# Performance work log

Hardware: AMD Instinct MI355X
Metric: run time of the kernel (lower is better)

The kernel has to match this reference:

```python
import jax, jax.numpy as jnp
import numpy as np

N, E = 100000, 600000
IN, HID, OUT, ED = 128, 128, 64, 32


def _gine_conv(x, src, dst, edge_feats, We, be, Wa, ba, Wb, bb):
    # GINEConv: msg = relu(x_j + Linear(edge_attr)); out = MLP((1+eps)*x + sum msg), eps=0
    e = edge_feats @ We + be                      # [E, C]
    msg = jax.nn.relu(x[src] + e)                 # gather + edge-add
    agg = jax.ops.segment_sum(msg, dst, num_segments=x.shape[0])
    h = x + agg                                   # eps = 0
    return jax.nn.relu(h @ Wa + ba) @ Wb + bb     # 2-layer MLP


def setup_inputs() -> dict:
    key = jax.random.key(0)
    ks = jax.random.split(key, 20)
    g = lambda k, shp, fan: jax.random.normal(k, shp, jnp.float32) * (1.0 / np.sqrt(fan))
    return {
        "x": jax.random.normal(ks[0], (N, IN), jnp.float32),
        "edge_index": jax.random.randint(ks[1], (2, E), 0, N, dtype=jnp.int32),
        "edge_feats": jax.random.normal(ks[2], (E, ED), jnp.float32),
        # conv1: edge lin (ED->IN), nn1 (IN->HID->HID)
        "We1": g(ks[3], (ED, IN), ED), "be1": jnp.zeros((IN,), jnp.float32),
        "W1a": g(ks[4], (IN, HID), IN), "b1a": jnp.zeros((HID,), jnp.float32),
        "W1b": g(ks[5], (HID, HID), HID), "b1b": jnp.zeros((HID,), jnp.float32),
        # conv2: edge lin (ED->HID), nn2 (HID->HID->HID)
        "We2": g(ks[6], (ED, HID), ED), "be2": jnp.zeros((HID,), jnp.float32),
        "W2a": g(ks[7], (HID, HID), HID), "b2a": jnp.zeros((HID,), jnp.float32),
        "W2b": g(ks[8], (HID, HID), HID), "b2b": jnp.zeros((HID,), jnp.float32),
        # heads
        "Wfc1": g(ks[9], (HID, HID), HID), "bfc1": jnp.zeros((HID,), jnp.float32),
        "Wfc2": g(ks[10], (HID, OUT), HID), "bfc2": jnp.zeros((OUT,), jnp.float32),
    }


def reference(x, edge_index, edge_feats,
              We1, be1, W1a, b1a, W1b, b1b,
              We2, be2, W2a, b2a, W2b, b2b,
              Wfc1, bfc1, Wfc2, bfc2):
    src, dst = edge_index[0], edge_index[1]  # source_to_target flow
    h = _gine_conv(x, src, dst, edge_feats, We1, be1, W1a, b1a, W1b, b1b)
    h = jnp.tanh(h)                          # dropout: eval-mode identity
    h = _gine_conv(h, src, dst, edge_feats, We2, be2, W2a, b2a, W2b, b2b)
    h = jnp.tanh(h)
    h = jnp.tanh(h @ Wfc1 + bfc1)
    return h @ Wfc2 + bfc2
```

## Files before the change

kernel.cpp:

```cpp
#include <hip/hip_runtime.h>
#include <hip/hip_fp16.h>
#include <math.h>

#define N_NODES 100000
#define N_EDGES 600000
#define NB_SCAN ((N_NODES + 1023) / 1024)

typedef unsigned short u16;
typedef __bf16 bf16x8 __attribute__((ext_vector_type(8)));
typedef float  f32x4  __attribute__((ext_vector_type(4)));

__device__ __forceinline__ u16 f2bf(float f) {
    union { float f; unsigned u; } c; c.f = f;
    unsigned u = c.u + 0x7fffu + ((c.u >> 16) & 1u);
    return (u16)(u >> 16);
}
__device__ __forceinline__ float bf2f(u16 h) {
    union { unsigned u; float f; } c; c.u = ((unsigned)h) << 16;
    return c.f;
}
__device__ __forceinline__ float fast_tanh(float x) {
    float e = __expf(2.0f * x);
    return 1.0f - 2.0f * __builtin_amdgcn_rcpf(e + 1.0f);
}

__global__ void hist_k(const int* __restrict__ dst, int* __restrict__ counts,
                       int* __restrict__ rank)
{
    int e = blockIdx.x * 256 + threadIdx.x;
    if (e < N_EDGES) rank[e] = atomicAdd(&counts[dst[e]], 1);
}

__global__ void scan_a_k(const int* __restrict__ counts, int* __restrict__ row_ptr,
                         int* __restrict__ blockSums)
{
    __shared__ int s[256];
    const int t = threadIdx.x;
    const int base = blockIdx.x * 1024 + t * 4;
    int c[4];
#pragma unroll
    for (int j = 0; j < 4; ++j) c[j] = (base + j < N_NODES) ? counts[base + j] : 0;
    const int tot = c[0] + c[1] + c[2] + c[3];
    s[t] = tot;
    __syncthreads();
    for (int off = 1; off < 256; off <<= 1) {
        int v = (t >= off) ? s[t - off] : 0;
        __syncthreads();
        s[t] += v;
        __syncthreads();
    }
    int run = s[t] - tot;
#pragma unroll
    for (int j = 0; j < 4; ++j) {
        if (base + j < N_NODES) row_ptr[base + j] = run;
        run += c[j];
    }
    if (t == 255) blockSums[blockIdx.x] = s[255];
}

__global__ void scan_b_k(const int* __restrict__ blockSums, int* __restrict__ blockOffs)
{
    if (threadIdx.x == 0) {
        int run = 0;
        for (int b = 0; b < NB_SCAN; ++b) { blockOffs[b] = run; run += blockSums[b]; }
    }
}

__global__ void scan_c_k(int* __restrict__ row_ptr, const int* __restrict__ blockOffs)
{
    int i = blockIdx.x * 256 + threadIdx.x;
    if (i < N_NODES) row_ptr[i] += blockOffs[i >> 10];
    if (i == 0) row_ptr[N_NODES] = N_EDGES;
}

__global__ void scatter_k(const int* __restrict__ src, const int* __restrict__ dst,
                          const int* __restrict__ row_ptr, const int* __restrict__ rank,
                          int* __restrict__ perm, int* __restrict__ src_sorted,
                          int* __restrict__ dst_sorted)
{
    int e = blockIdx.x * 256 + threadIdx.x;
    if (e < N_EDGES) {
        int pos = row_ptr[dst[e]] + rank[e];
        perm[pos] = e;
        src_sorted[pos] = src[e];
        dst_sorted[pos] = dst[e];
    }
}

__global__ void nzero_k(const int* __restrict__ row_ptr, float* __restrict__ agg)
{
    const int idx = blockIdx.x * 256 + threadIdx.x;
    const int n = idx >> 5;
    if (n >= N_NODES) return;
    const int rs = row_ptr[n], re = row_ptr[n + 1];
    const bool interior = (rs < re) && ((rs >> 6) == ((re - 1) >> 6));
    if (!interior) {
        const int c = (idx & 31) * 4;
        *(float4*)(agg + (size_t)n * 128 + c) = make_float4(0.f, 0.f, 0.f, 0.f);
    }
}

__global__ void wprep_k(const float* __restrict__ W1a, const float* __restrict__ W1b,
                        const float* __restrict__ W2a, const float* __restrict__ W2b,
                        const float* __restrict__ Wf1, const float* __restrict__ Wf2,
                        const float* __restrict__ We1, const float* __restrict__ We2,
                        u16* __restrict__ wT)
{
    int idx = blockIdx.x * 256 + threadIdx.x;
    if (idx >= 98304) return;
    if (idx >= 90112) {
        int l = idx - 90112;
        const int m = l >> 12;
        l &= 4095;
        const float* src = m ? We2 : We1;
        const int k = l >> 7, n = l & 127;
        const float w = src[k * 128 + n];
        const u16 hi = f2bf(w);
        const u16 lo = f2bf(w - bf2f(hi));
        const int base = 180224 + m * 8192;
        wT[base + n * 32 + k]        = hi;
        wT[base + 4096 + n * 32 + k] = lo;
        return;
    }
    int m, local;
    if      (idx < 16384) { m = 0; local = idx; }
    else if (idx < 32768) { m = 1; local = idx - 16384; }
    else if (idx < 49152) { m = 2; local = idx - 32768; }
    else if (idx < 65536) { m = 3; local = idx - 49152; }
    else if (idx < 81920) { m = 4; local = idx - 65536; }
    else                  { m = 5; local = idx - 81920; }
    const int N = (m == 5) ? 64 : 128;
    const float* src = (m == 0) ? W1a : (m == 1) ? W1b : (m == 2) ? W2a
                     : (m == 3) ? W2b : (m == 4) ? Wf1 : Wf2;
    const int k = local / N, n = local % N;
    const float w = src[k * N + n];
    const u16 hi = f2bf(w);
    const u16 lo = f2bf(w - bf2f(hi));
    const int base = m * 32768;
    const int sz   = (m == 5) ? 8192 : 16384;
    wT[base + n * 128 + k]      = hi;
    wT[base + sz + n * 128 + k] = lo;
}

__global__ __launch_bounds__(256, 6) void fused_conv_k(
    const float* __restrict__ x, const float* __restrict__ ef,
    const int* __restrict__ perm, const int* __restrict__ src_s,
    const int* __restrict__ dst_s, const int* __restrict__ row_ptr,
    const u16* __restrict__ WeT_hi, const u16* __restrict__ WeT_lo,
    const float* __restrict__ be, float* __restrict__ agg)
{
    __shared__ __align__(16) char smem[16896];
    u16 (*efHi)[40]  = (u16 (*)[40])smem;
    u16 (*efLo)[40]  = (u16 (*)[40])(smem + 5120);
    u16 (*msg16)[132] = (u16 (*)[132])smem;
    __shared__ int sSrc[64];
    __shared__ int sDst[64];

    const int t  = threadIdx.x;
    const int i0 = blockIdx.x * 64;

    if (t < 64) { sSrc[t] = src_s[i0 + t]; sDst[t] = dst_s[i0 + t]; }
    {
        const int row = t >> 2;
        const int q   = t & 3;
        const int e   = perm[i0 + row];
        const float* p = ef + (size_t)e * 32 + q * 8;
        const float4 v0 = *(const float4*)(p);
        const float4 v1 = *(const float4*)(p + 4);
        const float vv[8] = {v0.x, v0.y, v0.z, v0.w, v1.x, v1.y, v1.z, v1.w};
        unsigned hp[4], lp[4];
#pragma unroll
        for (int i = 0; i < 4; ++i) {
            const u16 h0 = f2bf(vv[2 * i]),     h1 = f2bf(vv[2 * i + 1]);
            const u16 l0 = f2bf(vv[2 * i]     - bf2f(h0));
            const u16 l1 = f2bf(vv[2 * i + 1] - bf2f(h1));
            hp[i] = (unsigned)h0 | ((unsigned)h1 << 16);
            lp[i] = (unsigned)l0 | ((unsigned)l1 << 16);
        }
        *(uint4*)&efHi[row][q * 8] = make_uint4(hp[0], hp[1], hp[2], hp[3]);
        *(uint4*)&efLo[row][q * 8] = make_uint4(lp[0], lp[1], lp[2], lp[3]);
    }
    __syncthreads();

    const int lane = t & 63, wave = t >> 6;
    const int quad = lane >> 4, col = lane & 15;

    bf16x8 bHi[2], bLo[2];
#pragma unroll
    for (int j = 0; j < 2; ++j) {
        const int nt = wave * 2 + j;
        const size_t off = (size_t)(nt * 16 + col) * 32 + quad * 8;
        bHi[j] = *(const bf16x8*)(WeT_hi + off);
        bLo[j] = *(const bf16x8*)(WeT_lo + off);
    }

    float xv[2][4][4];
#pragma unroll
    for (int m = 0; m < 4; ++m)
#pragma unroll
        for (int r = 0; r < 4; ++r) {
            const int s = sSrc[m * 16 + quad * 4 + r];
            const float* xp = x + (size_t)s * 128 + wave * 32 + col;
            xv[0][m][r] = xp[0];
            xv[1][m][r] = xp[16];
        }

    f32x4 acc[2][4];
#pragma unroll
    for (int j = 0; j < 2; ++j) {
        const float bv = be[wave * 32 + j * 16 + col];
#pragma unroll
        for (int m = 0; m < 4; ++m) acc[j][m] = (f32x4){bv, bv, bv, bv};
    }
#pragma unroll
    for (int m = 0; m < 4; ++m) {
        const bf16x8 aHi = *(const bf16x8*)&efHi[m * 16 + col][quad * 8];
        const bf16x8 aLo = *(const bf16x8*)&efLo[m * 16 + col][quad * 8];
#pragma unroll
        for (int j = 0; j < 2; ++j) {
            acc[j][m] = __builtin_amdgcn_mfma_f32_16x16x32_bf16(aHi, bHi[j], acc[j][m], 0, 0, 0);
            acc[j][m] = __builtin_amdgcn_mfma_f32_16x16x32_bf16(aHi, bLo[j], acc[j][m], 0, 0, 0);
            acc[j][m] = __builtin_amdgcn_mfma_f32_16x16x32_bf16(aLo, bHi[j], acc[j][m], 0, 0, 0);
        }
    }

#pragma unroll
    for (int j = 0; j < 2; ++j)
#pragma unroll
        for (int m = 0; m < 4; ++m)
#pragma unroll
            for (int r = 0; r < 4; ++r)
                acc[j][m][r] = fmaxf(acc[j][m][r] + xv[j][m][r], 0.f);

    __syncthreads();
#pragma unroll
    for (int j = 0; j < 2; ++j)
#pragma unroll
        for (int m = 0; m < 4; ++m)
#pragma unroll
            for (int r = 0; r < 4; ++r) {
                const __half hv = __float2half_rn(acc[j][m][r]);
                msg16[m * 16 + quad * 4 + r][wave * 32 + j * 16 + col] =
                    *(const u16*)&hv;
            }
    __syncthreads();

    const int c2 = lane * 2;
    const int nF = sDst[0], nL = sDst[63];
    for (int n = nF + wave; n <= nL; n += 4) {
        const int rs = row_ptr[n];
        const int re = row_ptr[n + 1];
        const int lo = rs > i0 ? rs : i0;
        const int hi = re < i0 + 64 ? re : i0 + 64;
        float a0 = 0.f, a1 = 0.f;
        for (int i = lo; i < hi; ++i) {
            const __half2 v = *(const __half2*)(&msg16[i - i0][c2]);
            const float2 f = __half22float2(v);
            a0 += f.x; a1 += f.y;
        }
        float* dp = agg + (size_t)n * 128 + c2;
        const bool interior = (rs >= i0) && (re <= i0 + 64);
        if (interior) {
            *(float2*)dp = make_float2(a0, a1);
        } else if (hi > lo) {
            atomicAdd(dp,     a0);
            atomicAdd(dp + 1, a1);
        }
    }
}

template <int NT2, bool TANH1, bool TANHF, bool ADDAGG>
__global__ __launch_bounds__(256, 4) void mlp2_mfma_k(
    const float* __restrict__ xin, const float* __restrict__ agg,
    const u16* __restrict__ WaT_hi, const u16* __restrict__ WaT_lo,
    const float* __restrict__ ba,
    const u16* __restrict__ WbT_hi, const u16* __restrict__ WbT_lo,
    const float* __restrict__ bb,
    float* __restrict__ out)
{
    __shared__ u16 sHi[64][136];
    __shared__ u16 sLo[64][136];
    const int tid = threadIdx.x;
    const int n0  = blockIdx.x * 64;

    {
        const int mrow = tid >> 5, kq = tid & 31;
#pragma unroll
        for (int g = 0; g < 8; ++g) {
            const int row  = g * 8 + mrow;
            const int node = n0 + row;
            float4 v = make_float4(0.f, 0.f, 0.f, 0.f);
            if (node < N_NODES) {
                v = *(const float4*)(xin + (size_t)node * 128 + kq * 4);
                if (ADDAGG) {
                    float4 a4 = *(const float4*)(agg + (size_t)node * 128 + kq * 4);
                    v.x += a4.x; v.y += a4.y; v.z += a4.z; v.w += a4.w;
                }
            }
            const u16 h0 = f2bf(v.x), h1 = f2bf(v.y), h2 = f2bf(v.z), h3 = f2bf(v.w);
            const u16 l0 = f2bf(v.x - bf2f(h0)), l1 = f2bf(v.y - bf2f(h1));
            const u16 l2 = f2bf(v.z - bf2f(h2)), l3 = f2bf(v.w - bf2f(h3));
            *(uint2*)&sHi[row][kq * 4] =
                make_uint2((unsigned)h0 | ((unsigned)h1 << 16), (unsigned)h2 | ((unsigned)h3 << 16));
            *(uint2*)&sLo[row][kq * 4] =
                make_uint2((unsigned)l0 | ((unsigned)l1 << 16), (unsigned)l2 | ((unsigned)l3 << 16));
        }
    }
    __syncthreads();

    const int lane = tid & 63, wave = tid >> 6;
    const int quad = lane >> 4, col = lane & 15;

    f32x4 accA[2][4];
#pragma unroll
    for (int j = 0; j < 2; ++j) {
        const int nt = wave * 2 + j;
        const float bv = ba[nt * 16 + col];
#pragma unroll
        for (int m = 0; m < 4; ++m) accA[j][m] = (f32x4){bv, bv, bv, bv};

        bf16x8 bHi[4], bLo[4];
#pragma unroll
        for (int k0 = 0; k0 < 4; ++k0) {
            const size_t off = (size_t)(nt * 16 + col) * 128 + k0 * 32 + quad * 8;
            bHi[k0] = *(const bf16x8*)(WaT_hi + off);
            bLo[k0] = *(const bf16x8*)(WaT_lo + off);
        }
#pragma unroll 2
        for (int m = 0; m < 4; ++m) {
#pragma unroll
            for (int k0 = 0; k0 < 4; ++k0) {
                const bf16x8 aHi = *(const bf16x8*)&sHi[m * 16 + col][k0 * 32 + quad * 8];
                const bf16x8 aLo = *(const bf16x8*)&sLo[m * 16 + col][k0 * 32 + quad * 8];
                accA[j][m] = __builtin_amdgcn_mfma_f32_16x16x32_bf16(aHi, bHi[k0], accA[j][m], 0, 0, 0);
                accA[j][m] = __builtin_amdgcn_mfma_f32_16x16x32_bf16(aHi, bLo[k0], accA[j][m], 0, 0, 0);
                accA[j][m] = __builtin_amdgcn_mfma_f32_16x16x32_bf16(aLo, bHi[k0], accA[j][m], 0, 0, 0);
            }
        }
    }
    __syncthreads();

#pragma unroll
    for (int j = 0; j < 2; ++j) {
        const int ct = (wave * 2 + j) * 16 + col;
#pragma unroll
        for (int m = 0; m < 4; ++m) {
#pragma unroll
            for (int r = 0; r < 4; ++r) {
                float v = TANH1 ? fast_tanh(accA[j][m][r]) : fmaxf(accA[j][m][r], 0.f);
                const u16 hv = f2bf(v);
                const u16 lv = f2bf(v - bf2f(hv));
                const int row = m * 16 + quad * 4 + r;
                sHi[row][ct] = hv;
                sLo[row][ct] = lv;
            }
        }
    }
    __syncthreads();

    constexpr int JB   = NT2 / 4;
    constexpr int NOUT = NT2 * 16;
#pragma unroll
    for (int j = 0; j < JB; ++j) {
        const int nt = wave * JB + j;
        const float bv = bb[nt * 16 + col];
        f32x4 accB[4];
#pragma unroll
        for (int m = 0; m < 4; ++m) accB[m] = (f32x4){bv, bv, bv, bv};

        bf16x8 bHi[4], bLo[4];
#pragma unroll
        for (int k0 = 0; k0 < 4; ++k0) {
            const size_t off = (size_t)(nt * 16 + col) * 128 + k0 * 32 + quad * 8;
            bHi[k0] = *(const bf16x8*)(WbT_hi + off);
            bLo[k0] = *(const bf16x8*)(WbT_lo + off);
        }
#pragma unroll 2
        for (int m = 0; m < 4; ++m) {
#pragma unroll
            for (int k0 = 0; k0 < 4; ++k0) {
                const bf16x8 tHi = *(const bf16x8*)&sHi[m * 16 + col][k0 * 32 + quad * 8];
                const bf16x8 tLo = *(const bf16x8*)&sLo[m * 16 + col][k0 * 32 + quad * 8];
                accB[m] = __builtin_amdgcn_mfma_f32_16x16x32_bf16(tHi, bHi[k0], accB[m], 0, 0, 0);
                accB[m] = __builtin_amdgcn_mfma_f32_16x16x32_bf16(tHi, bLo[k0], accB[m], 0, 0, 0);
                accB[m] = __builtin_amdgcn_mfma_f32_16x16x32_bf16(tLo, bHi[k0], accB[m], 0, 0, 0);
            }
        }
#pragma unroll
        for (int m = 0; m < 4; ++m) {
#pragma unroll
            for (int r = 0; r < 4; ++r) {
                const int node = n0 + m * 16 + quad * 4 + r;
                if (node < N_NODES) {
                    float v = accB[m][r];
                    if (TANHF) v = fast_tanh(v);
                    out[(size_t)node * NOUT + nt * 16 + col] = v;
                }
            }
        }
    }
}

__global__ __launch_bounds__(256, 4) void mlp4_mfma_k(
    const float* __restrict__ xin, const float* __restrict__ agg,
    const u16* __restrict__ W0hi, const u16* __restrict__ W0lo, const float* __restrict__ b0,
    const u16* __restrict__ W1hi, const u16* __restrict__ W1lo, const float* __restrict__ b1,
    const u16* __restrict__ W2hi, const u16* __restrict__ W2lo, const float* __restrict__ b2,
    const u16* __restrict__ W3hi, const u16* __restrict__ W3lo, const float* __restrict__ b3,
    float* __restrict__ out)
{
    __shared__ u16 sHi[64][136];
    __shared__ u16 sLo[64][136];
    const int tid = threadIdx.x;
    const int n0  = blockIdx.x * 64;

    {
        const int mrow = tid >> 5, kq = tid & 31;
#pragma unroll
        for (int g = 0; g < 8; ++g) {
            const int row  = g * 8 + mrow;
            const int node = n0 + row;
            float4 v = make_float4(0.f, 0.f, 0.f, 0.f);
            if (node < N_NODES) {
                v = *(const float4*)(xin + (size_t)node * 128 + kq * 4);
                float4 a4 = *(const float4*)(agg + (size_t)node * 128 + kq * 4);
                v.x += a4.x; v.y += a4.y; v.z += a4.z; v.w += a4.w;
            }
            const u16 h0 = f2bf(v.x), h1 = f2bf(v.y), h2 = f2bf(v.z), h3 = f2bf(v.w);
            const u16 l0 = f2bf(v.x - bf2f(h0)), l1 = f2bf(v.y - bf2f(h1));
            const u16 l2 = f2bf(v.z - bf2f(h2)), l3 = f2bf(v.w - bf2f(h3));
            *(uint2*)&sHi[row][kq * 4] =
                make_uint2((unsigned)h0 | ((unsigned)h1 << 16), (unsigned)h2 | ((unsigned)h3 << 16));
            *(uint2*)&sLo[row][kq * 4] =
                make_uint2((unsigned)l0 | ((unsigned)l1 << 16), (unsigned)l2 | ((unsigned)l3 << 16));
        }
    }
    __syncthreads();

    const int lane = tid & 63, wave = tid >> 6;
    const int quad = lane >> 4, col = lane & 15;

#pragma unroll 1
    for (int l = 0; l < 3; ++l) {
        const u16*   Whi = (l == 0) ? W0hi : (l == 1) ? W1hi : W2hi;
        const u16*   Wlo = (l == 0) ? W0lo : (l == 1) ? W1lo : W2lo;
        const float* bs  = (l == 0) ? b0   : (l == 1) ? b1   : b2;

        f32x4 acc[2][4];
#pragma unroll
        for (int j = 0; j < 2; ++j) {
            const int nt = wave * 2 + j;
            const float bv = bs[nt * 16 + col];
#pragma unroll
            for (int m = 0; m < 4; ++m) acc[j][m] = (f32x4){bv, bv, bv, bv};

            bf16x8 bHi[4], bLo[4];
#pragma unroll
            for (int k0 = 0; k0 < 4; ++k0) {
                const size_t off = (size_t)(nt * 16 + col) * 128 + k0 * 32 + quad * 8;
                bHi[k0] = *(const bf16x8*)(Whi + off);
                bLo[k0] = *(const bf16x8*)(Wlo + off);
            }
#pragma unroll 2
            for (int m = 0; m < 4; ++m) {
#pragma unroll
                for (int k0 = 0; k0 < 4; ++k0) {
                    const bf16x8 aHi = *(const bf16x8*)&sHi[m * 16 + col][k0 * 32 + quad * 8];
                    const bf16x8 aLo = *(const bf16x8*)&sLo[m * 16 + col][k0 * 32 + quad * 8];
                    acc[j][m] = __builtin_amdgcn_mfma_f32_16x16x32_bf16(aHi, bHi[k0], acc[j][m], 0, 0, 0);
                    acc[j][m] = __builtin_amdgcn_mfma_f32_16x16x32_bf16(aHi, bLo[k0], acc[j][m], 0, 0, 0);
                    acc[j][m] = __builtin_amdgcn_mfma_f32_16x16x32_bf16(aLo, bHi[k0], acc[j][m], 0, 0, 0);
                }
            }
        }
        __syncthreads();

#pragma unroll
        for (int j = 0; j < 2; ++j) {
            const int ct = (wave * 2 + j) * 16 + col;
#pragma unroll
            for (int m = 0; m < 4; ++m) {
#pragma unroll
                for (int r = 0; r < 4; ++r) {
                    float v = (l == 0) ? fmaxf(acc[j][m][r], 0.f)
                                       : fast_tanh(acc[j][m][r]);
                    const u16 hv = f2bf(v);
                    const u16 lv = f2bf(v - bf2f(hv));
                    const int row = m * 16 + quad * 4 + r;
                    sHi[row][ct] = hv;
                    sLo[row][ct] = lv;
                }
            }
        }
        __syncthreads();
    }

    {
        const int nt = wave;
        const float bv = b3[nt * 16 + col];
        f32x4 acc[4];
#pragma unroll
        for (int m = 0; m < 4; ++m) acc[m] = (f32x4){bv, bv, bv, bv};

        bf16x8 bHi[4], bLo[4];
#pragma unroll
        for (int k0 = 0; k0 < 4; ++k0) {
            const size_t off = (size_t)(nt * 16 + col) * 128 + k0 * 32 + quad * 8;
            bHi[k0] = *(const bf16x8*)(W3hi + off);
            bLo[k0] = *(const bf16x8*)(W3lo + off);
        }
#pragma unroll 2
        for (int m = 0; m < 4; ++m) {
#pragma unroll
            for (int k0 = 0; k0 < 4; ++k0) {
                const bf16x8 tHi = *(const bf16x8*)&sHi[m * 16 + col][k0 * 32 + quad * 8];
                const bf16x8 tLo = *(const bf16x8*)&sLo[m * 16 + col][k0 * 32 + quad * 8];
                acc[m] = __builtin_amdgcn_mfma_f32_16x16x32_bf16(tHi, bHi[k0], acc[m], 0, 0, 0);
                acc[m] = __builtin_amdgcn_mfma_f32_16x16x32_bf16(tHi, bLo[k0], acc[m], 0, 0, 0);
                acc[m] = __builtin_amdgcn_mfma_f32_16x16x32_bf16(tLo, bHi[k0], acc[m], 0, 0, 0);
            }
        }
#pragma unroll
        for (int m = 0; m < 4; ++m) {
#pragma unroll
            for (int r = 0; r < 4; ++r) {
                const int node = n0 + m * 16 + quad * 4 + r;
                if (node < N_NODES)
                    out[(size_t)node * 64 + nt * 16 + col] = acc[m][r];
            }
        }
    }
}

extern "C" void kernel_launch(void* const* d_in, const int* in_sizes, int n_in,
                              void* d_out, int out_size, void* d_ws, size_t ws_size,
                              hipStream_t stream)
{
    const float* x   = (const float*)d_in[0];
    const int*   ei  = (const int*)  d_in[1];
    const float* ef  = (const float*)d_in[2];
    const float* We1 = (const float*)d_in[3];
    const float* be1 = (const float*)d_in[4];
    const float* W1a = (const float*)d_in[5];
    const float* b1a = (const float*)d_in[6];
    const float* W1b = (const float*)d_in[7];
    const float* b1b = (const float*)d_in[8];
    const float* We2 = (const float*)d_in[9];
    const float* be2 = (const float*)d_in[10];
    const float* W2a = (const float*)d_in[11];
    const float* b2a = (const float*)d_in[12];
    const float* W2b = (const float*)d_in[13];
    const float* b2b = (const float*)d_in[14];
    const float* Wf1 = (const float*)d_in[15];
    const float* bf1 = (const float*)d_in[16];
    const float* Wf2 = (const float*)d_in[17];
    const float* bf2 = (const float*)d_in[18];
    float* out = (float*)d_out;

    const int* src = ei;
    const int* dst = ei + N_EDGES;

    float*  agg     = (float*)d_ws;
    float*  h       = agg + (size_t)N_NODES * 128;
    int*    row_ptr = (int*)(h + (size_t)N_NODES * 128);
    int*    perm    = row_ptr + (N_NODES + 8);
    int*    src_s   = perm + N_EDGES;
    int*    dst_srt = src_s + N_EDGES;
    u16*    wT      = (u16*)(dst_srt + N_EDGES);
    int* counts    = (int*)agg;
    int* rank      = counts + N_NODES;
    int* blockSums = rank + N_EDGES;
    int* blockOffs = blockSums + NB_SCAN;

    u16* W1aT = wT;
    u16* W1bT = wT + 32768;
    u16* W2aT = wT + 65536;
    u16* W2bT = wT + 98304;
    u16* Wf1T = wT + 131072;
    u16* Wf2T = wT + 163840;
    u16* We1T = wT + 180224;
    u16* We2T = wT + 188416;

    const int mlpGrid = (N_NODES + 63) / 64;
    const int eGrid   = (N_EDGES + 255) / 256;
    const int nGrid   = (N_NODES + 255) / 256;
    const int fcGrid  = N_EDGES / 64;
    const int wpGrid  = (98304 + 255) / 256;
    const int nzGrid  = (N_NODES * 32 + 255) / 256;

    hipMemsetAsync(counts, 0, (size_t)N_NODES * sizeof(int), stream);
    hist_k   <<<eGrid,   256, 0, stream>>>(dst, counts, rank);
    wprep_k  <<<wpGrid,  256, 0, stream>>>(W1a, W1b, W2a, W2b, Wf1, Wf2, We1, We2, wT);
    scan_a_k <<<NB_SCAN, 256, 0, stream>>>(counts, row_ptr, blockSums);
    scan_b_k <<<1,        64, 0, stream>>>(blockSums, blockOffs);
    scan_c_k <<<nGrid,   256, 0, stream>>>(row_ptr, blockOffs);
    scatter_k<<<eGrid,   256, 0, stream>>>(src, dst, row_ptr, rank, perm, src_s, dst_srt);

    nzero_k<<<nzGrid, 256, 0, stream>>>(row_ptr, agg);
    fused_conv_k<<<fcGrid, 256, 0, stream>>>(x, ef, perm, src_s, dst_srt, row_ptr,
                                             We1T, We1T + 4096, be1, agg);
    mlp2_mfma_k<8, false, true, true><<<mlpGrid, 256, 0, stream>>>(
        x, agg, W1aT, W1aT + 16384, b1a, W1bT, W1bT + 16384, b1b, h);

    nzero_k<<<nzGrid, 256, 0, stream>>>(row_ptr, agg);
    fused_conv_k<<<fcGrid, 256, 0, stream>>>(h, ef, perm, src_s, dst_srt, row_ptr,
                                             We2T, We2T + 4096, be2, agg);
    mlp4_mfma_k<<<mlpGrid, 256, 0, stream>>>(
        h, agg,
        W2aT, W2aT + 16384, b2a,
        W2bT, W2bT + 16384, b2b,
        Wf1T, Wf1T + 16384, bf1,
        Wf2T, Wf2T + 8192,  bf2,
        out);
}
```

Baseline: 508.2 us.

## Fold residual x into aggregation buffer and pre-seed agg from MLP output

```diff
diff --git a/kernel.cpp b/kernel.cpp
--- a/kernel.cpp
+++ b/kernel.cpp
@@ -87,7 +87,8 @@
     }
 }
 
-__global__ void nzero_k(const int* __restrict__ row_ptr, float* __restrict__ agg)
+__global__ void npre_k(const int* __restrict__ row_ptr,
+                       const float* __restrict__ xin, float* __restrict__ agg)
 {
     const int idx = blockIdx.x * 256 + threadIdx.x;
     const int n = idx >> 5;
@@ -96,7 +97,8 @@
     const bool interior = (rs < re) && ((rs >> 6) == ((re - 1) >> 6));
     if (!interior) {
         const int c = (idx & 31) * 4;
-        *(float4*)(agg + (size_t)n * 128 + c) = make_float4(0.f, 0.f, 0.f, 0.f);
+        *(float4*)(agg + (size_t)n * 128 + c) =
+            *(const float4*)(xin + (size_t)n * 128 + c);
     }
 }
 
@@ -250,6 +252,7 @@
     for (int n = nF + wave; n <= nL; n += 4) {
         const int rs = row_ptr[n];
         const int re = row_ptr[n + 1];
+        const float2 xn = *(const float2*)(x + (size_t)n * 128 + c2);
         const int lo = rs > i0 ? rs : i0;
         const int hi = re < i0 + 64 ? re : i0 + 64;
         float a0 = 0.f, a1 = 0.f;
@@ -261,7 +264,7 @@
         float* dp = agg + (size_t)n * 128 + c2;
         const bool interior = (rs >= i0) && (re <= i0 + 64);
         if (interior) {
-            *(float2*)dp = make_float2(a0, a1);
+            *(float2*)dp = make_float2(xn.x + a0, xn.y + a1);
         } else if (hi > lo) {
             atomicAdd(dp,     a0);
             atomicAdd(dp + 1, a1);
@@ -269,20 +272,29 @@
     }
 }
 
-template <int NT2, bool TANH1, bool TANHF, bool ADDAGG>
 __global__ __launch_bounds__(256, 4) void mlp2_mfma_k(
-    const float* __restrict__ xin, const float* __restrict__ agg,
+    const float* __restrict__ agg_in, const int* __restrict__ row_ptr,
     const u16* __restrict__ WaT_hi, const u16* __restrict__ WaT_lo,
     const float* __restrict__ ba,
     const u16* __restrict__ WbT_hi, const u16* __restrict__ WbT_lo,
     const float* __restrict__ bb,
-    float* __restrict__ out)
+    float* __restrict__ h_out, float* __restrict__ agg_out)
 {
     __shared__ u16 sHi[64][136];
     __shared__ u16 sLo[64][136];
+    __shared__ int sFlag[64];
     const int tid = threadIdx.x;
     const int n0  = blockIdx.x * 64;
 
+    if (tid < 64) {
+        int flag = 1;
+        const int node = n0 + tid;
+        if (node < N_NODES) {
+            const int rs = row_ptr[node], re = row_ptr[node + 1];
+            flag = (rs < re) && ((rs >> 6) == ((re - 1) >> 6));
+        }
+        sFlag[tid] = flag;
+    }
     {
         const int mrow = tid >> 5, kq = tid & 31;
 #pragma unroll
@@ -290,13 +302,8 @@
             const int row  = g * 8 + mrow;
             const int node = n0 + row;
             float4 v = make_float4(0.f, 0.f, 0.f, 0.f);
-            if (node < N_NODES) {
-                v = *(const float4*)(xin + (size_t)node * 128 + kq * 4);
-                if (ADDAGG) {
-                    float4 a4 = *(const float4*)(agg + (size_t)node * 128 + kq * 4);
-                    v.x += a4.x; v.y += a4.y; v.z += a4.z; v.w += a4.w;
-                }
-            }
+            if (node < N_NODES)
+                v = *(const float4*)(agg_in + (size_t)node * 128 + kq * 4);
             const u16 h0 = f2bf(v.x), h1 = f2bf(v.y), h2 = f2bf(v.z), h3 = f2bf(v.w);
             const u16 l0 = f2bf(v.x - bf2f(h0)), l1 = f2bf(v.y - bf2f(h1));
             const u16 l2 = f2bf(v.z - bf2f(h2)), l3 = f2bf(v.w - bf2f(h3));
@@ -347,7 +354,7 @@
         for (int m = 0; m < 4; ++m) {
 #pragma unroll
             for (int r = 0; r < 4; ++r) {
-                float v = TANH1 ? fast_tanh(accA[j][m][r]) : fmaxf(accA[j][m][r], 0.f);
+                float v = fmaxf(accA[j][m][r], 0.f);
                 const u16 hv = f2bf(v);
                 const u16 lv = f2bf(v - bf2f(hv));
                 const int row = m * 16 + quad * 4 + r;
@@ -358,11 +365,9 @@
     }
     __syncthreads();
 
-    constexpr int JB   = NT2 / 4;
-    constexpr int NOUT = NT2 * 16;
-#pragma unroll
-    for (int j = 0; j < JB; ++j) {
-        const int nt = wave * JB + j;
+#pragma unroll
+    for (int j = 0; j < 2; ++j) {
+        const int nt = wave * 2 + j;
         const float bv = bb[nt * 16 + col];
         f32x4 accB[4];
 #pragma unroll
@@ -390,11 +395,13 @@
         for (int m = 0; m < 4; ++m) {
 #pragma unroll
             for (int r = 0; r < 4; ++r) {
-                const int node = n0 + m * 16 + quad * 4 + r;
+                const int row  = m * 16 + quad * 4 + r;
+                const int node = n0 + row;
                 if (node < N_NODES) {
-                    float v = accB[m][r];
-                    if (TANHF) v = fast_tanh(v);
-                    out[(size_t)node * NOUT + nt * 16 + col] = v;
+                    const float v = fast_tanh(accB[m][r]);
+                    const size_t o = (size_t)node * 128 + nt * 16 + col;
+                    h_out[o] = v;
+                    if (!sFlag[row]) agg_out[o] = v;
                 }
             }
         }
@@ -402,7 +409,7 @@
 }
 
 __global__ __launch_bounds__(256, 4) void mlp4_mfma_k(
-    const float* __restrict__ xin, const float* __restrict__ agg,
+    const float* __restrict__ agg,
     const u16* __restrict__ W0hi, const u16* __restrict__ W0lo, const float* __restrict__ b0,
     const u16* __restrict__ W1hi, const u16* __restrict__ W1lo, const float* __restrict__ b1,
     const u16* __restrict__ W2hi, const u16* __restrict__ W2lo, const float* __restrict__ b2,
@@ -421,11 +428,8 @@
             const int row  = g * 8 + mrow;
             const int node = n0 + row;
             float4 v = make_float4(0.f, 0.f, 0.f, 0.f);
-            if (node < N_NODES) {
-                v = *(const float4*)(xin + (size_t)node * 128 + kq * 4);
-                float4 a4 = *(const float4*)(agg + (size_t)node * 128 + kq * 4);
-                v.x += a4.x; v.y += a4.y; v.z += a4.z; v.w += a4.w;
-            }
+            if (node < N_NODES)
+                v = *(const float4*)(agg + (size_t)node * 128 + kq * 4);
             const u16 h0 = f2bf(v.x), h1 = f2bf(v.y), h2 = f2bf(v.z), h3 = f2bf(v.w);
             const u16 l0 = f2bf(v.x - bf2f(h0)), l1 = f2bf(v.y - bf2f(h1));
             const u16 l2 = f2bf(v.z - bf2f(h2)), l3 = f2bf(v.w - bf2f(h3));
@@ -596,17 +600,16 @@
     scan_c_k <<<nGrid,   256, 0, stream>>>(row_ptr, blockOffs);
     scatter_k<<<eGrid,   256, 0, stream>>>(src, dst, row_ptr, rank, perm, src_s, dst_srt);
 
-    nzero_k<<<nzGrid, 256, 0, stream>>>(row_ptr, agg);
+    npre_k<<<nzGrid, 256, 0, stream>>>(row_ptr, x, agg);
     fused_conv_k<<<fcGrid, 256, 0, stream>>>(x, ef, perm, src_s, dst_srt, row_ptr,
                                              We1T, We1T + 4096, be1, agg);
-    mlp2_mfma_k<8, false, true, true><<<mlpGrid, 256, 0, stream>>>(
-        x, agg, W1aT, W1aT + 16384, b1a, W1bT, W1bT + 16384, b1b, h);
-
-    nzero_k<<<nzGrid, 256, 0, stream>>>(row_ptr, agg);
+    mlp2_mfma_k<<<mlpGrid, 256, 0, stream>>>(
+        agg, row_ptr, W1aT, W1aT + 16384, b1a, W1bT, W1bT + 16384, b1b, h, agg);
+
     fused_conv_k<<<fcGrid, 256, 0, stream>>>(h, ef, perm, src_s, dst_srt, row_ptr,
                                              We2T, We2T + 4096, be2, agg);
     mlp4_mfma_k<<<mlpGrid, 256, 0, stream>>>(
-        h, agg,
+        agg,
         W2aT, W2aT + 16384, b2a,
         W2bT, W2bT + 16384, b2b,
         Wf1T, Wf1T + 16384, bf1,
```

After: 500.3 us. No clear change (-1.6%).
